# Optimization experiments

Measured on AMD Instinct MI355X. Metric: run time of the kernel, lower is better.

The kernel has to match this reference:

```python
import jax, jax.numpy as jnp
import numpy as np

N_VAR, N_CONS, E = 50000, 50000, 800000
F, FE, H, ITERS = 64, 8, 128, 2  # node feat, edge feat, hidden, gnn iterations


def _mlp(x, w1, b1, w2, b2):
    # MultilayerPerceptron([in, hidden, out]) = Linear -> ReLU -> Linear
    return jax.nn.relu(x @ w1 + b1) @ w2 + b2


def setup_inputs() -> dict:
    key = jax.random.key(0)
    ks = jax.random.split(key, 17)

    def w(k, shape, fan_in):
        return jax.random.normal(k, shape, jnp.float32) / np.sqrt(fan_in).astype(np.float32)

    msg_in = 2 * F + FE   # 136
    upd_in = 2 * F        # 128
    return {
        "var_feat": jax.random.normal(ks[0], (N_VAR, F), jnp.float32),
        "cons_feat": jax.random.normal(ks[1], (N_CONS, F), jnp.float32),
        "edge_feat": jax.random.normal(ks[2], (E, FE), jnp.float32),
        "edge_var": jax.random.randint(ks[3], (E,), 0, N_VAR),
        "edge_cons": jax.random.randint(ks[4], (E,), 0, N_CONS),
        # messenger MLP (note: original code uses var messenger for BOTH sides)
        "w_msg1": w(ks[5], (ITERS, msg_in, H), msg_in),
        "b_msg1": jnp.zeros((ITERS, H), jnp.float32),
        "w_msg2": w(ks[6], (ITERS, H, F), H),
        "b_msg2": jnp.zeros((ITERS, F), jnp.float32),
        # var update MLP
        "w_vupd1": w(ks[7], (ITERS, upd_in, H), upd_in),
        "b_vupd1": jnp.zeros((ITERS, H), jnp.float32),
        "w_vupd2": w(ks[8], (ITERS, H, F), H),
        "b_vupd2": jnp.zeros((ITERS, F), jnp.float32),
        # cons update MLP
        "w_cupd1": w(ks[9], (ITERS, upd_in, H), upd_in),
        "b_cupd1": jnp.zeros((ITERS, H), jnp.float32),
        "w_cupd2": w(ks[10], (ITERS, H, F), H),
        "b_cupd2": jnp.zeros((ITERS, F), jnp.float32),
    }


def reference(var_feat, cons_feat, edge_feat, edge_var, edge_cons,
              w_msg1, b_msg1, w_msg2, b_msg2,
              w_vupd1, b_vupd1, w_vupd2, b_vupd2,
              w_cupd1, b_cupd1, w_cupd2, b_cupd2):
    for i in range(ITERS):
        vs = var_feat[edge_var]    # [E, F] gather of var endpoint feats
        cs = cons_feat[edge_cons]  # [E, F] gather of cons endpoint feats
        # --- var-node message pass: (var_feat, neighbor cons_feat, edge_feat) ---
        m_v = _mlp(jnp.concatenate([vs, cs, edge_feat], axis=1),
                   w_msg1[i], b_msg1[i], w_msg2[i], b_msg2[i])        # [E, F]
        agg_v = jax.ops.segment_sum(m_v, edge_var, num_segments=N_VAR)  # zeros for isolated nodes
        new_var = _mlp(jnp.concatenate([var_feat, agg_v], axis=1),
                       w_vupd1[i], b_vupd1[i], w_vupd2[i], b_vupd2[i])
        # --- cons-node message pass (uses var messenger weights, as in source) ---
        m_c = _mlp(jnp.concatenate([cs, vs, edge_feat], axis=1),
                   w_msg1[i], b_msg1[i], w_msg2[i], b_msg2[i])        # [E, F]
        agg_c = jax.ops.segment_sum(m_c, edge_cons, num_segments=N_CONS)
        new_cons = _mlp(jnp.concatenate([cons_feat, agg_c], axis=1),
                        w_cupd1[i], b_cupd1[i], w_cupd2[i], b_cupd2[i])
        var_feat, cons_feat = new_var, new_cons
    return var_feat, cons_feat
```

## Files before the change

kernel.cpp:

```cpp
#include <hip/hip_runtime.h>

#define N_NODES 50000
#define E_EDGES 800000
#define F 64
#define FE 8
#define H 128
#define MSG_IN 136
#define XPAD 168
#define HPW 68
#define NXP 136

typedef short bf16x8 __attribute__((ext_vector_type(8)));
typedef float f32x4 __attribute__((ext_vector_type(4)));

__device__ __forceinline__ ushort f2bf(float f) {
  uint u = __float_as_uint(f);
  u = (u + 0x7FFFu + ((u >> 16) & 1u)) >> 16;
  return (ushort)u;
}
__device__ __forceinline__ uint pack2(float a, float b) {
  return (uint)f2bf(a) | ((uint)f2bf(b) << 16);
}
__device__ __forceinline__ void atomic_pk_add_bf16(ushort* addr, uint data) {
  asm volatile("global_atomic_pk_add_bf16 %0, %1, off" :: "v"(addr), "v"(data) : "memory");
}

__global__ __launch_bounds__(256)
void cvt_feats(const float* __restrict__ a, const float* __restrict__ b,
               ushort* __restrict__ oa, ushort* __restrict__ ob) {
  const int n4 = N_NODES * F / 4;
  for (int i = blockIdx.x * blockDim.x + threadIdx.x; i < n4; i += gridDim.x * blockDim.x) {
    const float4 va = ((const float4*)a)[i];
    const float4 vb = ((const float4*)b)[i];
    ((uint2*)oa)[i] = make_uint2(pack2(va.x, va.y), pack2(va.z, va.w));
    ((uint2*)ob)[i] = make_uint2(pack2(vb.x, vb.y), pack2(vb.z, vb.w));
  }
}

__global__ __launch_bounds__(256, 2)
void edge_pass_mfma(const ushort* __restrict__ vfeat, const ushort* __restrict__ cfeat,
                    const float* __restrict__ efeat,
                    const int* __restrict__ ev, const int* __restrict__ ec,
                    const float* __restrict__ w1, const float* __restrict__ b1,
                    const float* __restrict__ w2, const float* __restrict__ b2,
                    ushort* __restrict__ aggv, ushort* __restrict__ aggc)
{
  __shared__ __align__(16) ushort sX[64 * XPAD];
  __shared__ __align__(16) uint  sH[64 * HPW];
  __shared__ int sIv[64], sIc[64];

  const int t = threadIdx.x;
  const int wid = t >> 6, l15 = t & 15, hi = (t >> 4) & 3;
  const int eh = wid >> 1, fh = wid & 1;

  bf16x8 bf1[2][5];
  #pragma unroll
  for (int n = 0; n < 2; ++n) {
    const int col = wid * 32 + n * 16 + l15;
    #pragma unroll
    for (int kb = 0; kb < 5; ++kb)
      #pragma unroll
      for (int i = 0; i < 8; ++i) {
        const int kg = kb * 32 + hi * 8 + i;
        bf1[n][kb][i] = (short)((kg < MSG_IN) ? f2bf(w1[kg * H + col]) : (ushort)0);
      }
  }
  bf16x8 bf2[2][4];
  #pragma unroll
  for (int fbl = 0; fbl < 2; ++fbl) {
    const int col = fh * 32 + 2 * l15 + fbl;
    #pragma unroll
    for (int kb = 0; kb < 4; ++kb)
      #pragma unroll
      for (int i = 0; i < 8; ++i) {
        const int p = hi * 8 + i;
        const int kl = (p >> 1) | ((p & 1) << 4);
        bf2[fbl][kb][i] = (short)f2bf(w2[(kb * 32 + kl) * F + col]);
      }
  }
  const float bb1[2] = { b1[wid * 32 + l15], b1[wid * 32 + 16 + l15] };
  const float bb2[2] = { b2[fh * 32 + 2 * l15], b2[fh * 32 + 2 * l15 + 1] };

  {
    uint* xu = (uint*)sX;
    for (int i = t; i < 64 * 16; i += 256) {
      const int row = i >> 4, u = i & 15;
      xu[row * (XPAD / 2) + 68 + u] = 0;
    }
  }

  const int r = t >> 2, q = t & 3;
  const int g = gridDim.x;
  const int nTiles = E_EDGES / 64;
  int tile = blockIdx.x;
  int ivC = ev[tile * 64 + r], icC = ec[tile * 64 + r];

  constexpr int perm[5] = {2, 3, 0, 1, 4};

  for (; tile < nTiles; tile += g) {
    {
      const uint4* vp = (const uint4*)(vfeat + (size_t)ivC * F);
      const uint4* cp = (const uint4*)(cfeat + (size_t)icC * F);
      uint4* xr4 = (uint4*)((uint*)sX + r * (XPAD / 2));
      xr4[q * 2]     = vp[q * 2];
      xr4[q * 2 + 1] = vp[q * 2 + 1];
      xr4[8 + q * 2]     = cp[q * 2];
      xr4[8 + q * 2 + 1] = cp[q * 2 + 1];
      if (q == 0) {
        const float4* ep = (const float4*)(efeat + (size_t)(tile * 64 + r) * FE);
        const float4 e0 = ep[0], e1 = ep[1];
        xr4[16] = make_uint4(pack2(e0.x, e0.y), pack2(e0.z, e0.w),
                             pack2(e1.x, e1.y), pack2(e1.z, e1.w));
      }
    }
    const int nt2 = (tile + g < nTiles) ? tile + g : tile;
    const int ivN = ev[nt2 * 64 + r];
    const int icN = ec[nt2 * 64 + r];
    __syncthreads();
    if (q == 0) { sIv[r] = ivC; sIc[r] = icC; }

    f32x4 aV[4][2], aC[4][2];
    #pragma unroll
    for (int m = 0; m < 4; ++m)
      #pragma unroll
      for (int n = 0; n < 2; ++n) { aV[m][n] = (f32x4)(0.f); aC[m][n] = (f32x4)(0.f); }

    #pragma unroll
    for (int kb = 0; kb < 5; ++kb)
      #pragma unroll
      for (int m = 0; m < 4; ++m) {
        const bf16x8 a = *(const bf16x8*)&sX[(m * 16 + l15) * XPAD + kb * 32 + hi * 8];
        #pragma unroll
        for (int n = 0; n < 2; ++n) {
          aV[m][n] = __builtin_amdgcn_mfma_f32_16x16x32_bf16(a, bf1[n][kb],       aV[m][n], 0, 0, 0);
          aC[m][n] = __builtin_amdgcn_mfma_f32_16x16x32_bf16(a, bf1[n][perm[kb]], aC[m][n], 0, 0, 0);
        }
      }

    uint pC[4][4];
    #pragma unroll
    for (int m = 0; m < 4; ++m)
      #pragma unroll
      for (int rr = 0; rr < 4; ++rr) {
        const int e = m * 16 + hi * 4 + rr;
        sH[e * HPW + wid * 16 + l15] =
            pack2(fmaxf(aV[m][0][rr] + bb1[0], 0.f), fmaxf(aV[m][1][rr] + bb1[1], 0.f));
        pC[m][rr] =
            pack2(fmaxf(aC[m][0][rr] + bb1[0], 0.f), fmaxf(aC[m][1][rr] + bb1[1], 0.f));
      }
    __syncthreads();

    const ushort* sHu = (const ushort*)sH;
    {
      f32x4 a2[2][2];
      #pragma unroll
      for (int mm = 0; mm < 2; ++mm) { a2[mm][0] = (f32x4)(0.f); a2[mm][1] = (f32x4)(0.f); }
      #pragma unroll
      for (int kb = 0; kb < 4; ++kb)
        #pragma unroll
        for (int mm = 0; mm < 2; ++mm) {
          const int e = (eh * 2 + mm) * 16 + l15;
          const bf16x8 a = *(const bf16x8*)&sHu[e * (HPW * 2) + kb * 32 + hi * 8];
          a2[mm][0] = __builtin_amdgcn_mfma_f32_16x16x32_bf16(a, bf2[0][kb], a2[mm][0], 0, 0, 0);
          a2[mm][1] = __builtin_amdgcn_mfma_f32_16x16x32_bf16(a, bf2[1][kb], a2[mm][1], 0, 0, 0);
        }
      #pragma unroll
      for (int mm = 0; mm < 2; ++mm)
        #pragma unroll
        for (int rr = 0; rr < 4; ++rr) {
          const int idx = sIv[(eh * 2 + mm) * 16 + hi * 4 + rr];
          ushort* dst = aggv + (size_t)idx * F + fh * 32 + 2 * l15;
          atomic_pk_add_bf16(dst, pack2(a2[mm][0][rr] + bb2[0], a2[mm][1][rr] + bb2[1]));
        }
    }
    __syncthreads();

    #pragma unroll
    for (int m = 0; m < 4; ++m)
      #pragma unroll
      for (int rr = 0; rr < 4; ++rr)
        sH[(m * 16 + hi * 4 + rr) * HPW + wid * 16 + l15] = pC[m][rr];
    __syncthreads();

    {
      f32x4 a2[2][2];
      #pragma unroll
      for (int mm = 0; mm < 2; ++mm) { a2[mm][0] = (f32x4)(0.f); a2[mm][1] = (f32x4)(0.f); }
      #pragma unroll
      for (int kb = 0; kb < 4; ++kb)
        #pragma unroll
        for (int mm = 0; mm < 2; ++mm) {
          const int e = (eh * 2 + mm) * 16 + l15;
          const bf16x8 a = *(const bf16x8*)&sHu[e * (HPW * 2) + kb * 32 + hi * 8];
          a2[mm][0] = __builtin_amdgcn_mfma_f32_16x16x32_bf16(a, bf2[0][kb], a2[mm][0], 0, 0, 0);
          a2[mm][1] = __builtin_amdgcn_mfma_f32_16x16x32_bf16(a, bf2[1][kb], a2[mm][1], 0, 0, 0);
        }
      #pragma unroll
      for (int mm = 0; mm < 2; ++mm)
        #pragma unroll
        for (int rr = 0; rr < 4; ++rr) {
          const int idx = sIc[(eh * 2 + mm) * 16 + hi * 4 + rr];
          ushort* dst = aggc + (size_t)idx * F + fh * 32 + 2 * l15;
          atomic_pk_add_bf16(dst, pack2(a2[mm][0][rr] + bb2[0], a2[mm][1][rr] + bb2[1]));
        }
    }
    ivC = ivN; icC = icN;
  }
}

__global__ __launch_bounds__(256, 2)
void node_update_dual(ushort* __restrict__ vfeat, const ushort* __restrict__ vagg,
                      ushort* __restrict__ cfeat, const ushort* __restrict__ cagg,
                      const float* __restrict__ w1v, const float* __restrict__ b1v,
                      const float* __restrict__ w2v, const float* __restrict__ b2v,
                      const float* __restrict__ w1c, const float* __restrict__ b1c,
                      const float* __restrict__ w2c, const float* __restrict__ b2c,
                      float* __restrict__ outv, float* __restrict__ outc,
                      int writeF32)
{
  __shared__ __align__(16) ushort sX[64 * NXP];
  __shared__ __align__(16) uint  sH[64 * HPW];

  const int half = (N_NODES + 63) / 64;
  const bool isC = (int)blockIdx.x >= half;
  const int tile = isC ? blockIdx.x - half : blockIdx.x;
  ushort* feat = isC ? cfeat : vfeat;
  const ushort* agg = isC ? cagg : vagg;
  const float* w1 = isC ? w1c : w1v;  const float* b1 = isC ? b1c : b1v;
  const float* w2 = isC ? w2c : w2v;  const float* b2 = isC ? b2c : b2v;
  float* outf = isC ? outc : outv;

  const int t = threadIdx.x;
  const int wid = t >> 6, l15 = t & 15, hi = (t >> 4) & 3;

  bf16x8 bf1[2][4];
  #pragma unroll
  for (int n = 0; n < 2; ++n) {
    const int col = wid * 32 + n * 16 + l15;
    #pragma unroll
    for (int kb = 0; kb < 4; ++kb)
      #pragma unroll
      for (int i = 0; i < 8; ++i)
        bf1[n][kb][i] = (short)f2bf(w1[(kb * 32 + hi * 8 + i) * H + col]);
  }
  bf16x8 bf2[2][2][4];
  #pragma unroll
  for (int gg = 0; gg < 2; ++gg)
    #pragma unroll
    for (int fbl = 0; fbl < 2; ++fbl) {
      const int col = gg * 32 + 2 * l15 + fbl;
      #pragma unroll
      for (int kb = 0; kb < 4; ++kb)
        #pragma unroll
        for (int i = 0; i < 8; ++i) {
          const int p = hi * 8 + i;
          const int kl = (p >> 1) | ((p & 1) << 4);
          bf2[gg][fbl][kb][i] = (short)f2bf(w2[(kb * 32 + kl) * F + col]);
        }
    }
  const float bb1[2] = { b1[wid * 32 + l15], b1[wid * 32 + 16 + l15] };
  float bb2[2][2];
  #pragma unroll
  for (int gg = 0; gg < 2; ++gg) {
    bb2[gg][0] = b2[gg * 32 + 2 * l15];
    bb2[gg][1] = b2[gg * 32 + 2 * l15 + 1];
  }

  const int r = t >> 2, q = t & 3;
  {
    const int node = tile * 64 + r;
    const int nc = node < N_NODES ? node : N_NODES - 1;
    const uint4* fp = (const uint4*)(feat + (size_t)nc * F);
    const uint4* ap = (const uint4*)(agg + (size_t)nc * F);
    uint4* xr4 = (uint4*)&sX[r * NXP];
    xr4[q * 2]     = fp[q * 2];
    xr4[q * 2 + 1] = fp[q * 2 + 1];
    xr4[8 + q * 2]     = ap[q * 2];
    xr4[8 + q * 2 + 1] = ap[q * 2 + 1];
  }
  __syncthreads();

  f32x4 aV[4][2];
  #pragma unroll
  for (int m = 0; m < 4; ++m)
    #pragma unroll
    for (int n = 0; n < 2; ++n) aV[m][n] = (f32x4)(0.f);
  #pragma unroll
  for (int kb = 0; kb < 4; ++kb)
    #pragma unroll
    for (int m = 0; m < 4; ++m) {
      const bf16x8 a = *(const bf16x8*)&sX[(m * 16 + l15) * NXP + kb * 32 + hi * 8];
      #pragma unroll
      for (int n = 0; n < 2; ++n)
        aV[m][n] = __builtin_amdgcn_mfma_f32_16x16x32_bf16(a, bf1[n][kb], aV[m][n], 0, 0, 0);
    }
  #pragma unroll
  for (int m = 0; m < 4; ++m)
    #pragma unroll
    for (int rr = 0; rr < 4; ++rr) {
      const int e = m * 16 + hi * 4 + rr;
      sH[e * HPW + wid * 16 + l15] =
          pack2(fmaxf(aV[m][0][rr] + bb1[0], 0.f), fmaxf(aV[m][1][rr] + bb1[1], 0.f));
    }
  __syncthreads();

  f32x4 a2[2][2];
  #pragma unroll
  for (int gg = 0; gg < 2; ++gg)
    #pragma unroll
    for (int fbl = 0; fbl < 2; ++fbl) a2[gg][fbl] = (f32x4)(0.f);
  const ushort* sHu = (const ushort*)sH;
  #pragma unroll
  for (int kb = 0; kb < 4; ++kb) {
    const int e = wid * 16 + l15;
    const bf16x8 a = *(const bf16x8*)&sHu[e * (HPW * 2) + kb * 32 + hi * 8];
    #pragma unroll
    for (int gg = 0; gg < 2; ++gg)
      #pragma unroll
      for (int fbl = 0; fbl < 2; ++fbl)
        a2[gg][fbl] = __builtin_amdgcn_mfma_f32_16x16x32_bf16(a, bf2[gg][fbl][kb], a2[gg][fbl], 0, 0, 0);
  }
  #pragma unroll
  for (int rr = 0; rr < 4; ++rr) {
    const int node = tile * 64 + wid * 16 + hi * 4 + rr;
    if (node < N_NODES) {
      #pragma unroll
      for (int gg = 0; gg < 2; ++gg) {
        const float o0 = a2[gg][0][rr] + bb2[gg][0];
        const float o1 = a2[gg][1][rr] + bb2[gg][1];
        *(uint*)&feat[(size_t)node * F + gg * 32 + 2 * l15] = pack2(o0, o1);
        if (writeF32) {
          float2 o = make_float2(o0, o1);
          *(float2*)&outf[(size_t)node * F + gg * 32 + 2 * l15] = o;
        }
      }
    }
  }
}

extern "C" void kernel_launch(void* const* d_in, const int* in_sizes, int n_in,
                              void* d_out, int out_size, void* d_ws, size_t ws_size,
                              hipStream_t stream) {
  const float* var_feat  = (const float*)d_in[0];
  const float* cons_feat = (const float*)d_in[1];
  const float* edge_feat = (const float*)d_in[2];
  const int*   ev        = (const int*)d_in[3];
  const int*   ec        = (const int*)d_in[4];
  const float* w_msg1  = (const float*)d_in[5];
  const float* b_msg1  = (const float*)d_in[6];
  const float* w_msg2  = (const float*)d_in[7];
  const float* b_msg2  = (const float*)d_in[8];
  const float* w_vupd1 = (const float*)d_in[9];
  const float* b_vupd1 = (const float*)d_in[10];
  const float* w_vupd2 = (const float*)d_in[11];
  const float* b_vupd2 = (const float*)d_in[12];
  const float* w_cupd1 = (const float*)d_in[13];
  const float* b_cupd1 = (const float*)d_in[14];
  const float* w_cupd2 = (const float*)d_in[15];
  const float* b_cupd2 = (const float*)d_in[16];

  const size_t NF = (size_t)N_NODES * F;
  ushort* aggv = (ushort*)d_ws;
  ushort* aggc = aggv + NF;
  ushort* vb   = aggc + NF;
  ushort* cb   = vb + NF;
  float* outv = (float*)d_out;
  float* outc = outv + NF;

  cvt_feats<<<512, 256, 0, stream>>>(var_feat, cons_feat, vb, cb);

  for (int it = 0; it < 2; ++it) {
    hipMemsetAsync(aggv, 0, 2 * NF * sizeof(ushort), stream);

    edge_pass_mfma<<<1024, 256, 0, stream>>>(vb, cb, edge_feat, ev, ec,
        w_msg1 + (size_t)it * MSG_IN * H, b_msg1 + (size_t)it * H,
        w_msg2 + (size_t)it * H * F,      b_msg2 + (size_t)it * F,
        aggv, aggc);

    node_update_dual<<<1564, 256, 0, stream>>>(vb, aggv, cb, aggc,
        w_vupd1 + (size_t)it * H * H, b_vupd1 + (size_t)it * H,
        w_vupd2 + (size_t)it * H * F, b_vupd2 + (size_t)it * F,
        w_cupd1 + (size_t)it * H * H, b_cupd1 + (size_t)it * H,
        w_cupd2 + (size_t)it * H * F, b_cupd2 + (size_t)it * F,
        outv, outc, it == 1 ? 1 : 0);
  }
}
```

Measured before the change: 493.8 us.

## Fold first-layer bias into padded K column, reuse one accumulator, raise occupancy

```diff
diff --git a/kernel.cpp b/kernel.cpp
--- a/kernel.cpp
+++ b/kernel.cpp
@@ -18,8 +18,10 @@
   u = (u + 0x7FFFu + ((u >> 16) & 1u)) >> 16;
   return (ushort)u;
 }
-__device__ __forceinline__ uint pack2(float a, float b) {
-  return (uint)f2bf(a) | ((uint)f2bf(b) << 16);
+__device__ __forceinline__ uint pack2(float lo, float hi) {
+  uint r;
+  asm("v_cvt_pk_bf16_f32 %0, %1, %2" : "=v"(r) : "v"(lo), "v"(hi));
+  return r;
 }
 __device__ __forceinline__ void atomic_pk_add_bf16(ushort* addr, uint data) {
   asm volatile("global_atomic_pk_add_bf16 %0, %1, off" :: "v"(addr), "v"(data) : "memory");
@@ -37,7 +39,7 @@
   }
 }
 
-__global__ __launch_bounds__(256, 2)
+__global__ __launch_bounds__(256, 3)
 void edge_pass_mfma(const ushort* __restrict__ vfeat, const ushort* __restrict__ cfeat,
                     const float* __restrict__ efeat,
                     const int* __restrict__ ev, const int* __restrict__ ec,
@@ -62,7 +64,10 @@
       #pragma unroll
       for (int i = 0; i < 8; ++i) {
         const int kg = kb * 32 + hi * 8 + i;
-        bf1[n][kb][i] = (short)((kg < MSG_IN) ? f2bf(w1[kg * H + col]) : (ushort)0);
+        float val = 0.f;
+        if (kg < MSG_IN) val = w1[kg * H + col];
+        else if (kg == MSG_IN) val = b1[col];
+        bf1[n][kb][i] = (short)f2bf(val);
       }
   }
   bf16x8 bf2[2][4];
@@ -78,14 +83,13 @@
         bf2[fbl][kb][i] = (short)f2bf(w2[(kb * 32 + kl) * F + col]);
       }
   }
-  const float bb1[2] = { b1[wid * 32 + l15], b1[wid * 32 + 16 + l15] };
   const float bb2[2] = { b2[fh * 32 + 2 * l15], b2[fh * 32 + 2 * l15 + 1] };
 
   {
     uint* xu = (uint*)sX;
     for (int i = t; i < 64 * 16; i += 256) {
       const int row = i >> 4, u = i & 15;
-      xu[row * (XPAD / 2) + 68 + u] = 0;
+      xu[row * (XPAD / 2) + 68 + u] = (u == 0) ? 0x00003F80u : 0u;
     }
   }
 
@@ -119,38 +123,32 @@
     __syncthreads();
     if (q == 0) { sIv[r] = ivC; sIc[r] = icC; }
 
-    f32x4 aV[4][2], aC[4][2];
+    f32x4 acc[4][2];
+    const ushort* sHu = (const ushort*)sH;
+
     #pragma unroll
     for (int m = 0; m < 4; ++m)
       #pragma unroll
-      for (int n = 0; n < 2; ++n) { aV[m][n] = (f32x4)(0.f); aC[m][n] = (f32x4)(0.f); }
-
+      for (int n = 0; n < 2; ++n) acc[m][n] = (f32x4)(0.f);
     #pragma unroll
     for (int kb = 0; kb < 5; ++kb)
       #pragma unroll
       for (int m = 0; m < 4; ++m) {
         const bf16x8 a = *(const bf16x8*)&sX[(m * 16 + l15) * XPAD + kb * 32 + hi * 8];
         #pragma unroll
-        for (int n = 0; n < 2; ++n) {
-          aV[m][n] = __builtin_amdgcn_mfma_f32_16x16x32_bf16(a, bf1[n][kb],       aV[m][n], 0, 0, 0);
-          aC[m][n] = __builtin_amdgcn_mfma_f32_16x16x32_bf16(a, bf1[n][perm[kb]], aC[m][n], 0, 0, 0);
-        }
-      }
-
-    uint pC[4][4];
+        for (int n = 0; n < 2; ++n)
+          acc[m][n] = __builtin_amdgcn_mfma_f32_16x16x32_bf16(a, bf1[n][kb], acc[m][n], 0, 0, 0);
+      }
     #pragma unroll
     for (int m = 0; m < 4; ++m)
       #pragma unroll
       for (int rr = 0; rr < 4; ++rr) {
         const int e = m * 16 + hi * 4 + rr;
         sH[e * HPW + wid * 16 + l15] =
-            pack2(fmaxf(aV[m][0][rr] + bb1[0], 0.f), fmaxf(aV[m][1][rr] + bb1[1], 0.f));
-        pC[m][rr] =
-            pack2(fmaxf(aC[m][0][rr] + bb1[0], 0.f), fmaxf(aC[m][1][rr] + bb1[1], 0.f));
+            pack2(fmaxf(acc[m][0][rr], 0.f), fmaxf(acc[m][1][rr], 0.f));
       }
     __syncthreads();
 
-    const ushort* sHu = (const ushort*)sH;
     {
       f32x4 a2[2][2];
       #pragma unroll
@@ -173,13 +171,29 @@
           atomic_pk_add_bf16(dst, pack2(a2[mm][0][rr] + bb2[0], a2[mm][1][rr] + bb2[1]));
         }
     }
+
+    #pragma unroll
+    for (int m = 0; m < 4; ++m)
+      #pragma unroll
+      for (int n = 0; n < 2; ++n) acc[m][n] = (f32x4)(0.f);
+    #pragma unroll
+    for (int kb = 0; kb < 5; ++kb)
+      #pragma unroll
+      for (int m = 0; m < 4; ++m) {
+        const bf16x8 a = *(const bf16x8*)&sX[(m * 16 + l15) * XPAD + kb * 32 + hi * 8];
+        #pragma unroll
+        for (int n = 0; n < 2; ++n)
+          acc[m][n] = __builtin_amdgcn_mfma_f32_16x16x32_bf16(a, bf1[n][perm[kb]], acc[m][n], 0, 0, 0);
+      }
     __syncthreads();
-
     #pragma unroll
     for (int m = 0; m < 4; ++m)
       #pragma unroll
-      for (int rr = 0; rr < 4; ++rr)
-        sH[(m * 16 + hi * 4 + rr) * HPW + wid * 16 + l15] = pC[m][rr];
+      for (int rr = 0; rr < 4; ++rr) {
+        const int e = m * 16 + hi * 4 + rr;
+        sH[e * HPW + wid * 16 + l15] =
+            pack2(fmaxf(acc[m][0][rr], 0.f), fmaxf(acc[m][1][rr], 0.f));
+      }
     __syncthreads();
 
     {
```

New measurement: 488.9 us. Within noise of the previous version (-1.0%).
